# Performance work log

Measured on AMD Instinct MI355X. Metric: run time of the kernel, lower is better.

## Reference

```python
import jax, jax.numpy as jnp
import numpy as np

IN_CH = 512
HID = 512
SCALE = 1.0 / np.sqrt(16.0)  # hard-coded 16**0.5 in source, not sqrt(hidden)


def setup_inputs() -> dict:
    key = jax.random.key(0)
    ks = jax.random.split(key, 9)
    B, T = 8, 2048
    lim = 1.0 / np.sqrt(IN_CH)
    return {
        "q": jax.random.normal(ks[0], (B, T, IN_CH), dtype=jnp.float32),
        "k": jax.random.normal(ks[1], (B, T, IN_CH), dtype=jnp.float32),
        "v": jax.random.normal(ks[2], (B, T, IN_CH), dtype=jnp.float32),
        "Wq": jax.random.uniform(ks[3], (IN_CH, HID), jnp.float32, -lim, lim),
        "bq": jax.random.uniform(ks[4], (HID,), jnp.float32, -lim, lim),
        "Wk": jax.random.uniform(ks[5], (IN_CH, HID), jnp.float32, -lim, lim),
        "bk": jax.random.uniform(ks[6], (HID,), jnp.float32, -lim, lim),
        "Wv": jax.random.uniform(ks[7], (IN_CH, HID), jnp.float32, -lim, lim),
        "bv": jax.random.uniform(ks[8], (HID,), jnp.float32, -lim, lim),
    }


def reference(q, k, v, Wq, bq, Wk, bk, Wv, bv):
    # Linear projections: [B,T,F] @ [F,H] + [H]
    query = jnp.einsum("btf,fh->bth", q, Wq) + bq
    key_p = jnp.einsum("btf,fh->bth", k, Wk) + bk
    value = jnp.einsum("btf,fh->bth", v, Wv) + bv
    # energy: [B,T,T], scaled by fixed 1/sqrt(16)
    energy = jnp.einsum("bth,bsh->bts", query, key_p) * SCALE
    attn = jax.nn.softmax(energy, axis=-1)
    # weighted sum: [B,T,H]
    return jnp.einsum("bts,bsh->bth", attn, value)
```

## Files before the change

### kernel.cpp

```cpp
#include <hip/hip_runtime.h>
#include <stdint.h>

typedef __bf16 bf16;
typedef bf16 bf16x8 __attribute__((ext_vector_type(8)));
typedef float f32x4 __attribute__((ext_vector_type(4)));

#define MFMA(a, b, c) __builtin_amdgcn_mfma_f32_16x16x32_bf16(a, b, c, 0, 0, 0)

#define SCALE_L2E 0.3606737602222409f
#define M0 16.0f

__device__ __forceinline__ void gload_lds16(const void* g, void* l) {
  __builtin_amdgcn_global_load_lds(
      (const __attribute__((address_space(1))) uint32_t*)g,
      (__attribute__((address_space(3))) uint32_t*)l, 16, 0, 0);
}

__global__ void k_wtrans(const float* __restrict__ Wq, const float* __restrict__ Wk,
                         const float* __restrict__ Wv, bf16* __restrict__ Wt) {
  __shared__ float tile[32][33];
  int x = threadIdx.x, y = threadIdx.y;
  int k0 = blockIdx.x * 32, n0 = blockIdx.y * 32, z = blockIdx.z;
  const float* W = (z == 0) ? Wq : (z == 1) ? Wk : Wv;
  for (int j = 0; j < 4; j++)
    tile[y + 8 * j][x] = W[(size_t)(k0 + y + 8 * j) * 512 + n0 + x];
  __syncthreads();
  bf16* o = Wt + (size_t)z * 262144;
  for (int j = 0; j < 4; j++)
    o[(size_t)(n0 + y + 8 * j) * 512 + k0 + x] = (bf16)tile[x][y + 8 * j];
}

__global__ __launch_bounds__(256, 2) void k_proj(
    const float* __restrict__ q, const float* __restrict__ k, const float* __restrict__ v,
    const bf16* __restrict__ Wt, const float* __restrict__ bq, const float* __restrict__ bk,
    const float* __restrict__ bv, bf16* __restrict__ Qp, bf16* __restrict__ Kp,
    bf16* __restrict__ Vtp) {
  int z = blockIdx.z;
  const float* A = (z == 0) ? q : (z == 1) ? k : v;
  const float* bias = (z == 0) ? bq : (z == 1) ? bk : bv;
  const bf16* Bw = Wt + (size_t)z * 262144;

  int m0 = blockIdx.x * 128, n0 = blockIdx.y * 128;
  __shared__ __align__(16) char smem[65536];
  bf16* As = (bf16*)smem;
  bf16* Bs = (bf16*)(smem + 32768);
  bf16* Ts = (bf16*)smem;

  int tid = threadIdx.x;
  int wave = tid >> 6, lane = tid & 63, qr = lane & 15, quad = lane >> 4;
  int wm = (wave >> 1) * 64, wn = (wave & 1) * 64;

  f32x4 acc[4][4];
  for (int mi = 0; mi < 4; mi++)
    for (int ni = 0; ni < 4; ni++) acc[mi][ni] = (f32x4){0.f, 0.f, 0.f, 0.f};

  float4 rx[4], ry[4];

  auto issue = [&](int kk, int buf) {
#pragma unroll
    for (int i = 0; i < 4; i++) {
      int ch = i * 256 + tid, row = ch >> 3, c = ch & 7;
      const float4* src = (const float4*)(A + (size_t)(m0 + row) * 512 + kk + c * 8);
      rx[i] = src[0];
      ry[i] = src[1];
    }
#pragma unroll
    for (int i = 0; i < 4; i++) {
      int ch = i * 256 + tid, row = ch >> 3, c = ch & 7, cs = c ^ (row & 7);
      gload_lds16(Bw + (size_t)(n0 + row) * 512 + kk + cs * 8, &Bs[buf * 8192 + ch * 8]);
    }
  };

  auto writeA = [&](int buf) {
#pragma unroll
    for (int i = 0; i < 4; i++) {
      int ch = i * 256 + tid, row = ch >> 3, c = ch & 7, cs = c ^ (row & 7);
      bf16x8 t;
      t[0] = (bf16)rx[i].x; t[1] = (bf16)rx[i].y; t[2] = (bf16)rx[i].z; t[3] = (bf16)rx[i].w;
      t[4] = (bf16)ry[i].x; t[5] = (bf16)ry[i].y; t[6] = (bf16)ry[i].z; t[7] = (bf16)ry[i].w;
      *(bf16x8*)&As[buf * 8192 + row * 64 + cs * 8] = t;
    }
  };

  auto compute = [&](int buf) {
    bf16* Ab = &As[buf * 8192];
    bf16* Bb = &Bs[buf * 8192];
#pragma unroll
    for (int h = 0; h < 2; h++) {
      bf16x8 af[4], bfv[4];
#pragma unroll
      for (int mi = 0; mi < 4; mi++) {
        int rr = wm + mi * 16 + qr;
        int cc = (h * 4 + quad) ^ (rr & 7);
        af[mi] = *(bf16x8*)&Ab[rr * 64 + cc * 8];
      }
#pragma unroll
      for (int ni = 0; ni < 4; ni++) {
        int rr = wn + ni * 16 + qr;
        int cc = (h * 4 + quad) ^ (rr & 7);
        bfv[ni] = *(bf16x8*)&Bb[rr * 64 + cc * 8];
      }
#pragma unroll
      for (int mi = 0; mi < 4; mi++)
#pragma unroll
        for (int ni = 0; ni < 4; ni++) acc[mi][ni] = MFMA(af[mi], bfv[ni], acc[mi][ni]);
    }
  };

  issue(0, 0);
  writeA(0);
  __syncthreads();

  int cur = 0;
  for (int t = 0; t < 8; t++) {
    if (t < 7) issue((t + 1) * 64, cur ^ 1);
    compute(cur);
    if (t < 7) writeA(cur ^ 1);
    __syncthreads();
    cur ^= 1;
  }

  if (z == 2) {
    for (int ni = 0; ni < 4; ni++) {
      int hcol = wn + ni * 16 + qr;
      float bz = bias[n0 + hcol];
      for (int mi = 0; mi < 4; mi++) {
        int tl = wm + mi * 16 + quad * 4;
        bf16 tmp[4];
        for (int r = 0; r < 4; r++) tmp[r] = (bf16)(acc[mi][ni][r] + bz);
        *(uint64_t*)&Ts[hcol * 136 + tl] = *(uint64_t*)tmp;
      }
    }
    __syncthreads();
    int bb = m0 >> 11, t0l = m0 & 2047;
    for (int i = 0; i < 8; i++) {
      int ch = i * 256 + tid;
      int row = ch >> 4, c = ch & 15;
      *(bf16x8*)(Vtp + (size_t)(bb * 512 + n0 + row) * 2048 + t0l + c * 8) =
          *(bf16x8*)&Ts[row * 136 + c * 8];
    }
  } else {
    bf16* C = (z == 0) ? Qp : Kp;
    float sc = (z == 0) ? SCALE_L2E : 1.0f;
    for (int ni = 0; ni < 4; ni++) {
      int col = n0 + wn + ni * 16 + qr;
      float bz = bias[col];
      for (int mi = 0; mi < 4; mi++) {
        int rbase = m0 + wm + mi * 16 + quad * 4;
        for (int r = 0; r < 4; r++)
          C[(size_t)(rbase + r) * 512 + col] = (bf16)((acc[mi][ni][r] + bz) * sc);
      }
    }
  }
}

__global__ __launch_bounds__(256, 2) void k_qk(const bf16* __restrict__ Qp,
                                               const bf16* __restrict__ Kp,
                                               bf16* __restrict__ P,
                                               float* __restrict__ Lpart) {
  __shared__ bf16 As[2][128 * 64];
  __shared__ bf16 Bs[2][128 * 64];
  int b = blockIdx.z;
  const bf16* A = Qp + (size_t)b * 2048 * 512;
  const bf16* B = Kp + (size_t)b * 2048 * 512;
  bf16* Pb = P + (size_t)b * 2048 * 2048;
  int m0 = blockIdx.x * 128, n0 = blockIdx.y * 128;
  int tid = threadIdx.x;
  int wave = tid >> 6, lane = tid & 63, qr = lane & 15, quad = lane >> 4;
  int wm = (wave >> 1) * 64, wn = (wave & 1) * 64;

  f32x4 acc[4][4];
  for (int mi = 0; mi < 4; mi++)
    for (int ni = 0; ni < 4; ni++) acc[mi][ni] = (f32x4){0.f, 0.f, 0.f, 0.f};

  auto stage = [&](int kk, int buf) {
#pragma unroll
    for (int i = 0; i < 4; i++) {
      int ch = i * 256 + tid, row = ch >> 3, c = ch & 7, cs = c ^ (row & 7);
      gload_lds16(A + (size_t)(m0 + row) * 512 + kk + cs * 8, &As[buf][ch * 8]);
      gload_lds16(B + (size_t)(n0 + row) * 512 + kk + cs * 8, &Bs[buf][ch * 8]);
    }
  };

  auto compute = [&](int buf) {
#pragma unroll
    for (int h = 0; h < 2; h++) {
      bf16x8 af[4], bfv[4];
#pragma unroll
      for (int mi = 0; mi < 4; mi++) {
        int rr = wm + mi * 16 + qr;
        int cc = (h * 4 + quad) ^ (rr & 7);
        af[mi] = *(bf16x8*)&As[buf][rr * 64 + cc * 8];
      }
#pragma unroll
      for (int ni = 0; ni < 4; ni++) {
        int rr = wn + ni * 16 + qr;
        int cc = (h * 4 + quad) ^ (rr & 7);
        bfv[ni] = *(bf16x8*)&Bs[buf][rr * 64 + cc * 8];
      }
#pragma unroll
      for (int mi = 0; mi < 4; mi++)
#pragma unroll
        for (int ni = 0; ni < 4; ni++) acc[mi][ni] = MFMA(af[mi], bfv[ni], acc[mi][ni]);
    }
  };

  stage(0, 0);
  __syncthreads();
  int cur = 0;
  for (int t = 0; t < 8; t++) {
    if (t < 7) stage((t + 1) * 64, cur ^ 1);
    compute(cur);
    __syncthreads();
    cur ^= 1;
  }

  int slice = blockIdx.y * 2 + (wave & 1);
  float* Lp = Lpart + (size_t)slice * 16384 + b * 2048;
  for (int mi = 0; mi < 4; mi++) {
    int rowb = m0 + wm + mi * 16 + quad * 4;
    for (int r = 0; r < 4; r++) {
      float s = 0.f;
      bf16* prow = Pb + (size_t)(rowb + r) * 2048 + n0 + wn + qr;
      for (int ni = 0; ni < 4; ni++) {
        float e = exp2f(acc[mi][ni][r] - M0);
        prow[ni * 16] = (bf16)e;
        s += e;
      }
      s += __shfl_xor(s, 1);
      s += __shfl_xor(s, 2);
      s += __shfl_xor(s, 4);
      s += __shfl_xor(s, 8);
      if (qr == 0) Lp[rowb + r] = s;
    }
  }
}

__global__ __launch_bounds__(256, 2) void k_pv(const bf16* __restrict__ P,
                                               const bf16* __restrict__ Vtp,
                                               const float* __restrict__ Lpart,
                                               float* __restrict__ out) {
  __shared__ bf16 As[2][128 * 64];
  __shared__ bf16 Bs[2][128 * 64];
  int b = blockIdx.z;
  const bf16* A = P + (size_t)b * 2048 * 2048;
  const bf16* B = Vtp + (size_t)b * 512 * 2048;
  int m0 = blockIdx.x * 128, n0 = blockIdx.y * 128;
  int tid = threadIdx.x;
  int wave = tid >> 6, lane = tid & 63, qr = lane & 15, quad = lane >> 4;
  int wm = (wave >> 1) * 64, wn = (wave & 1) * 64;

  float linv_own = 0.f;
  if (tid < 128) {
    float s = 0.f;
    for (int j = 0; j < 32; j++) s += Lpart[(size_t)j * 16384 + b * 2048 + m0 + tid];
    linv_own = 1.0f / s;
  }

  f32x4 acc[4][4];
  for (int mi = 0; mi < 4; mi++)
    for (int ni = 0; ni < 4; ni++) acc[mi][ni] = (f32x4){0.f, 0.f, 0.f, 0.f};

  auto stage = [&](int kk, int buf) {
#pragma unroll
    for (int i = 0; i < 4; i++) {
      int ch = i * 256 + tid, row = ch >> 3, c = ch & 7, cs = c ^ (row & 7);
      gload_lds16(A + (size_t)(m0 + row) * 2048 + kk + cs * 8, &As[buf][ch * 8]);
      gload_lds16(B + (size_t)(n0 + row) * 2048 + kk + cs * 8, &Bs[buf][ch * 8]);
    }
  };

  auto compute = [&](int buf) {
#pragma unroll
    for (int h = 0; h < 2; h++) {
      bf16x8 af[4], bfv[4];
#pragma unroll
      for (int mi = 0; mi < 4; mi++) {
        int rr = wm + mi * 16 + qr;
        int cc = (h * 4 + quad) ^ (rr & 7);
        af[mi] = *(bf16x8*)&As[buf][rr * 64 + cc * 8];
      }
#pragma unroll
      for (int ni = 0; ni < 4; ni++) {
        int rr = wn + ni * 16 + qr;
        int cc = (h * 4 + quad) ^ (rr & 7);
        bfv[ni] = *(bf16x8*)&Bs[buf][rr * 64 + cc * 8];
      }
#pragma unroll
      for (int mi = 0; mi < 4; mi++)
#pragma unroll
        for (int ni = 0; ni < 4; ni++) acc[mi][ni] = MFMA(af[mi], bfv[ni], acc[mi][ni]);
    }
  };

  stage(0, 0);
  __syncthreads();
  int cur = 0;
  for (int t = 0; t < 32; t++) {
    if (t < 31) stage((t + 1) * 64, cur ^ 1);
    compute(cur);
    __syncthreads();
    cur ^= 1;
  }

  float* Linv_s = (float*)&As[0][0];
  if (tid < 128) Linv_s[tid] = linv_own;
  __syncthreads();

  for (int mi = 0; mi < 4; mi++) {
    int rowl = wm + mi * 16 + quad * 4;
    float linv[4];
    for (int r = 0; r < 4; r++) linv[r] = Linv_s[rowl + r];
    for (int ni = 0; ni < 4; ni++) {
      int col = n0 + wn + ni * 16 + qr;
      float* og = out + (size_t)(b * 2048 + m0 + rowl) * 512 + col;
      for (int r = 0; r < 4; r++) og[(size_t)r * 512] = acc[mi][ni][r] * linv[r];
    }
  }
}

extern "C" void kernel_launch(void* const* d_in, const int* in_sizes, int n_in,
                              void* d_out, int out_size, void* d_ws, size_t ws_size,
                              hipStream_t stream) {
  (void)in_sizes; (void)n_in; (void)out_size; (void)ws_size;
  const float* q  = (const float*)d_in[0];
  const float* k  = (const float*)d_in[1];
  const float* v  = (const float*)d_in[2];
  const float* Wq = (const float*)d_in[3];
  const float* bq = (const float*)d_in[4];
  const float* Wk = (const float*)d_in[5];
  const float* bk = (const float*)d_in[6];
  const float* Wv = (const float*)d_in[7];
  const float* bv = (const float*)d_in[8];
  float* out = (float*)d_out;

  char* ws = (char*)d_ws;
  bf16* Wt     = (bf16*)(ws);
  bf16* Qp     = (bf16*)(ws + 1572864);
  bf16* Kp     = (bf16*)(ws + 18350080);
  bf16* Vtp    = (bf16*)(ws + 35127296);
  bf16* P      = (bf16*)(ws + 51904512);
  float* Lpart = (float*)(ws + 119013376);

  k_wtrans<<<dim3(16, 16, 3), dim3(32, 8, 1), 0, stream>>>(Wq, Wk, Wv, Wt);
  k_proj<<<dim3(128, 4, 3), 256, 0, stream>>>(q, k, v, Wt, bq, bk, bv, Qp, Kp, Vtp);
  k_qk<<<dim3(16, 16, 8), 256, 0, stream>>>(Qp, Kp, P, Lpart);
  k_pv<<<dim3(16, 4, 8), 256, 0, stream>>>(P, Vtp, Lpart, out);
}
```

Before: 278.8 us.

## Enlarge QK and PV tiles to 8-wave blocks with explicit barrier-scheduled MFMA phases

The QK^T kernel moves from 128x128 to 256x256 output tiles and the PV kernel from 128x128 to 256x128, each using 512 threads (8 waves) and one block per CU. Each K-step splits into two MFMA phases. They are separated by explicit s_barrier and waitcnt, with sched_barrier and setprio raising wave priority during the matrix work. This replaces __syncthreads. The larger tiles aim to cut redundant global/L2 loads of Q, K, P and V, and the manual scheduling aims to overlap LDS reads, async global-to-LDS copies and MFMA. In exchange, LDS use grows to 128KB and 96KB, occupancy drops to one block per CU, and the PV grid shrinks to 256 blocks, which can hurt latency hiding and tail balance.

```diff
diff --git a/kernel.cpp b/kernel.cpp
--- a/kernel.cpp
+++ b/kernel.cpp
@@ -9,6 +9,12 @@
 
 #define SCALE_L2E 0.3606737602222409f
 #define M0 16.0f
+
+#define WAITVM0 asm volatile("s_waitcnt vmcnt(0)" ::: "memory")
+#define WAITLGKM0 asm volatile("s_waitcnt lgkmcnt(0)" ::: "memory")
+#define SBAR __builtin_amdgcn_s_barrier()
+#define SCHEDB __builtin_amdgcn_sched_barrier(0)
+#define PRIO(x) __builtin_amdgcn_s_setprio(x)
 
 __device__ __forceinline__ void gload_lds16(const void* g, void* l) {
   __builtin_amdgcn_global_load_lds(
@@ -154,74 +160,112 @@
   }
 }
 
-__global__ __launch_bounds__(256, 2) void k_qk(const bf16* __restrict__ Qp,
+__global__ __launch_bounds__(512, 1) void k_qk(const bf16* __restrict__ Qp,
                                                const bf16* __restrict__ Kp,
                                                bf16* __restrict__ P,
                                                float* __restrict__ Lpart) {
-  __shared__ bf16 As[2][128 * 64];
-  __shared__ bf16 Bs[2][128 * 64];
+  __shared__ __align__(16) bf16 S[65536];
   int b = blockIdx.z;
   const bf16* A = Qp + (size_t)b * 2048 * 512;
   const bf16* B = Kp + (size_t)b * 2048 * 512;
   bf16* Pb = P + (size_t)b * 2048 * 2048;
-  int m0 = blockIdx.x * 128, n0 = blockIdx.y * 128;
+  int m0 = blockIdx.x * 256, n0 = blockIdx.y * 256;
   int tid = threadIdx.x;
   int wave = tid >> 6, lane = tid & 63, qr = lane & 15, quad = lane >> 4;
-  int wm = (wave >> 1) * 64, wn = (wave & 1) * 64;
-
-  f32x4 acc[4][4];
-  for (int mi = 0; mi < 4; mi++)
+  int wm = wave >> 2, wn = wave & 3;
+
+  f32x4 acc[8][4];
+  for (int mi = 0; mi < 8; mi++)
     for (int ni = 0; ni < 4; ni++) acc[mi][ni] = (f32x4){0.f, 0.f, 0.f, 0.f};
 
-  auto stage = [&](int kk, int buf) {
-#pragma unroll
-    for (int i = 0; i < 4; i++) {
-      int ch = i * 256 + tid, row = ch >> 3, c = ch & 7, cs = c ^ (row & 7);
-      gload_lds16(A + (size_t)(m0 + row) * 512 + kk + cs * 8, &As[buf][ch * 8]);
-      gload_lds16(B + (size_t)(n0 + row) * 512 + kk + cs * 8, &Bs[buf][ch * 8]);
+  auto stage = [&](int t, int s) {
+    int kk = t * 64;
+    bf16* As_ = S + s * 16384;
+    bf16* Bs_ = S + 32768 + s * 16384;
+#pragma unroll
+    for (int j = 0; j < 4; j++) {
+      int ch = j * 512 + tid, row = ch >> 3, c = ch & 7, cs = c ^ (row & 7);
+      gload_lds16(A + (size_t)(m0 + row) * 512 + kk + cs * 8, As_ + ch * 8);
+    }
+#pragma unroll
+    for (int j = 0; j < 4; j++) {
+      int ch = j * 512 + tid, row = ch >> 3, c = ch & 7, cs = c ^ (row & 7);
+      gload_lds16(B + (size_t)(n0 + row) * 512 + kk + cs * 8, Bs_ + ch * 8);
     }
   };
 
-  auto compute = [&](int buf) {
-#pragma unroll
-    for (int h = 0; h < 2; h++) {
-      bf16x8 af[4], bfv[4];
-#pragma unroll
-      for (int mi = 0; mi < 4; mi++) {
-        int rr = wm + mi * 16 + qr;
-        int cc = (h * 4 + quad) ^ (rr & 7);
-        af[mi] = *(bf16x8*)&As[buf][rr * 64 + cc * 8];
-      }
-#pragma unroll
-      for (int ni = 0; ni < 4; ni++) {
-        int rr = wn + ni * 16 + qr;
-        int cc = (h * 4 + quad) ^ (rr & 7);
-        bfv[ni] = *(bf16x8*)&Bs[buf][rr * 64 + cc * 8];
-      }
+  stage(0, 0);
+  WAITVM0;
+  SBAR;
+
+  for (int t = 0; t < 8; t++) {
+    int cur = t & 1;
+    bf16* As_ = S + cur * 16384;
+    bf16* Bs_ = S + 32768 + cur * 16384;
+
+    if (t < 7) stage(t + 1, cur ^ 1);
+    bf16x8 aF[4][2], bF[4][2];
+#pragma unroll
+    for (int mi = 0; mi < 4; mi++)
+#pragma unroll
+      for (int kk = 0; kk < 2; kk++) {
+        int row = wm * 128 + mi * 16 + qr;
+        aF[mi][kk] = *(bf16x8*)&As_[row * 64 + ((kk * 4 + quad) ^ (row & 7)) * 8];
+      }
+#pragma unroll
+    for (int ni = 0; ni < 4; ni++)
+#pragma unroll
+      for (int kk = 0; kk < 2; kk++) {
+        int row = wn * 64 + ni * 16 + qr;
+        bF[ni][kk] = *(bf16x8*)&Bs_[row * 64 + ((kk * 4 + quad) ^ (row & 7)) * 8];
+      }
+    SBAR;
+    WAITLGKM0;
+    SCHEDB;
+    PRIO(1);
+#pragma unroll
+    for (int kk = 0; kk < 2; kk++)
 #pragma unroll
       for (int mi = 0; mi < 4; mi++)
 #pragma unroll
-        for (int ni = 0; ni < 4; ni++) acc[mi][ni] = MFMA(af[mi], bfv[ni], acc[mi][ni]);
-    }
-  };
-
-  stage(0, 0);
-  __syncthreads();
-  int cur = 0;
-  for (int t = 0; t < 8; t++) {
-    if (t < 7) stage((t + 1) * 64, cur ^ 1);
-    compute(cur);
-    __syncthreads();
-    cur ^= 1;
-  }
-
-  int slice = blockIdx.y * 2 + (wave & 1);
+        for (int ni = 0; ni < 4; ni++)
+          acc[mi][ni] = MFMA(aF[mi][kk], bF[ni][kk], acc[mi][ni]);
+    PRIO(0);
+    SBAR;
+
+#pragma unroll
+    for (int mi = 0; mi < 4; mi++)
+#pragma unroll
+      for (int kk = 0; kk < 2; kk++) {
+        int row = wm * 128 + 64 + mi * 16 + qr;
+        aF[mi][kk] = *(bf16x8*)&As_[row * 64 + ((kk * 4 + quad) ^ (row & 7)) * 8];
+      }
+    SBAR;
+    WAITLGKM0;
+    SCHEDB;
+    PRIO(1);
+#pragma unroll
+    for (int kk = 0; kk < 2; kk++)
+#pragma unroll
+      for (int mi = 0; mi < 4; mi++)
+#pragma unroll
+        for (int ni = 0; ni < 4; ni++)
+          acc[4 + mi][ni] = MFMA(aF[mi][kk], bF[ni][kk], acc[4 + mi][ni]);
+    PRIO(0);
+    WAITVM0;
+    SBAR;
+  }
+
+  int slice = blockIdx.y * 4 + wn;
   float* Lp = Lpart + (size_t)slice * 16384 + b * 2048;
-  for (int mi = 0; mi < 4; mi++) {
-    int rowb = m0 + wm + mi * 16 + quad * 4;
+#pragma unroll
+  for (int mi = 0; mi < 8; mi++) {
+    int rowb = m0 + wm * 128 + mi * 16 + quad * 4;
+#pragma unroll
     for (int r = 0; r < 4; r++) {
       float s = 0.f;
-      bf16* prow = Pb + (size_t)(rowb + r) * 2048 + n0 + wn + qr;
+      bf16* prow = Pb + (size_t)(rowb + r) * 2048 + n0 + wn * 64 + qr;
+#pragma unroll
       for (int ni = 0; ni < 4; ni++) {
         float e = exp2f(acc[mi][ni][r] - M0);
         prow[ni * 16] = (bf16)e;
@@ -236,22 +280,21 @@
   }
 }
 
-__global__ __launch_bounds__(256, 2) void k_pv(const bf16* __restrict__ P,
+__global__ __launch_bounds__(512, 1) void k_pv(const bf16* __restrict__ P,
                                                const bf16* __restrict__ Vtp,
                                                const float* __restrict__ Lpart,
                                                float* __restrict__ out) {
-  __shared__ bf16 As[2][128 * 64];
-  __shared__ bf16 Bs[2][128 * 64];
+  __shared__ __align__(16) bf16 S[49152];
   int b = blockIdx.z;
   const bf16* A = P + (size_t)b * 2048 * 2048;
   const bf16* B = Vtp + (size_t)b * 512 * 2048;
-  int m0 = blockIdx.x * 128, n0 = blockIdx.y * 128;
+  int m0 = blockIdx.x * 256, n0 = blockIdx.y * 128;
   int tid = threadIdx.x;
   int wave = tid >> 6, lane = tid & 63, qr = lane & 15, quad = lane >> 4;
-  int wm = (wave >> 1) * 64, wn = (wave & 1) * 64;
+  int wmi = wave >> 1, wni = wave & 1;
 
   float linv_own = 0.f;
-  if (tid < 128) {
+  if (tid < 256) {
     float s = 0.f;
     for (int j = 0; j < 32; j++) s += Lpart[(size_t)j * 16384 + b * 2048 + m0 + tid];
     linv_own = 1.0f / s;
@@ -261,58 +304,96 @@
   for (int mi = 0; mi < 4; mi++)
     for (int ni = 0; ni < 4; ni++) acc[mi][ni] = (f32x4){0.f, 0.f, 0.f, 0.f};
 
-  auto stage = [&](int kk, int buf) {
-#pragma unroll
-    for (int i = 0; i < 4; i++) {
-      int ch = i * 256 + tid, row = ch >> 3, c = ch & 7, cs = c ^ (row & 7);
-      gload_lds16(A + (size_t)(m0 + row) * 2048 + kk + cs * 8, &As[buf][ch * 8]);
-      gload_lds16(B + (size_t)(n0 + row) * 2048 + kk + cs * 8, &Bs[buf][ch * 8]);
+  auto stage = [&](int t, int s) {
+    int kk = t * 64;
+    bf16* As_ = S + s * 16384;
+    bf16* Bs_ = S + 32768 + s * 8192;
+#pragma unroll
+    for (int j = 0; j < 4; j++) {
+      int ch = j * 512 + tid, row = ch >> 3, c = ch & 7, cs = c ^ (row & 7);
+      gload_lds16(A + (size_t)(m0 + row) * 2048 + kk + cs * 8, As_ + ch * 8);
+    }
+#pragma unroll
+    for (int j = 0; j < 2; j++) {
+      int ch = j * 512 + tid, row = ch >> 3, c = ch & 7, cs = c ^ (row & 7);
+      gload_lds16(B + (size_t)(n0 + row) * 2048 + kk + cs * 8, Bs_ + ch * 8);
     }
   };
 
-  auto compute = [&](int buf) {
-#pragma unroll
-    for (int h = 0; h < 2; h++) {
-      bf16x8 af[4], bfv[4];
-#pragma unroll
-      for (int mi = 0; mi < 4; mi++) {
-        int rr = wm + mi * 16 + qr;
-        int cc = (h * 4 + quad) ^ (rr & 7);
-        af[mi] = *(bf16x8*)&As[buf][rr * 64 + cc * 8];
-      }
-#pragma unroll
-      for (int ni = 0; ni < 4; ni++) {
-        int rr = wn + ni * 16 + qr;
-        int cc = (h * 4 + quad) ^ (rr & 7);
-        bfv[ni] = *(bf16x8*)&Bs[buf][rr * 64 + cc * 8];
-      }
-#pragma unroll
-      for (int mi = 0; mi < 4; mi++)
-#pragma unroll
-        for (int ni = 0; ni < 4; ni++) acc[mi][ni] = MFMA(af[mi], bfv[ni], acc[mi][ni]);
-    }
-  };
-
   stage(0, 0);
-  __syncthreads();
-  int cur = 0;
+  WAITVM0;
+  SBAR;
+
   for (int t = 0; t < 32; t++) {
-    if (t < 31) stage((t + 1) * 64, cur ^ 1);
-    compute(cur);
-    __syncthreads();
-    cur ^= 1;
-  }
-
-  float* Linv_s = (float*)&As[0][0];
-  if (tid < 128) Linv_s[tid] = linv_own;
-  __syncthreads();
-
+    int cur = t & 1;
+    bf16* As_ = S + cur * 16384;
+    bf16* Bs_ = S + 32768 + cur * 8192;
+
+    if (t < 31) stage(t + 1, cur ^ 1);
+    bf16x8 aF[2][2], bF[4][2];
+#pragma unroll
+    for (int mi = 0; mi < 2; mi++)
+#pragma unroll
+      for (int kk = 0; kk < 2; kk++) {
+        int row = wmi * 64 + mi * 16 + qr;
+        aF[mi][kk] = *(bf16x8*)&As_[row * 64 + ((kk * 4 + quad) ^ (row & 7)) * 8];
+      }
+#pragma unroll
+    for (int ni = 0; ni < 4; ni++)
+#pragma unroll
+      for (int kk = 0; kk < 2; kk++) {
+        int row = wni * 64 + ni * 16 + qr;
+        bF[ni][kk] = *(bf16x8*)&Bs_[row * 64 + ((kk * 4 + quad) ^ (row & 7)) * 8];
+      }
+    SBAR;
+    WAITLGKM0;
+    SCHEDB;
+    PRIO(1);
+#pragma unroll
+    for (int kk = 0; kk < 2; kk++)
+#pragma unroll
+      for (int mi = 0; mi < 2; mi++)
+#pragma unroll
+        for (int ni = 0; ni < 4; ni++)
+          acc[mi][ni] = MFMA(aF[mi][kk], bF[ni][kk], acc[mi][ni]);
+    PRIO(0);
+    SBAR;
+
+#pragma unroll
+    for (int mi = 0; mi < 2; mi++)
+#pragma unroll
+      for (int kk = 0; kk < 2; kk++) {
+        int row = wmi * 64 + 32 + mi * 16 + qr;
+        aF[mi][kk] = *(bf16x8*)&As_[row * 64 + ((kk * 4 + quad) ^ (row & 7)) * 8];
+      }
+    SBAR;
+    WAITLGKM0;
+    SCHEDB;
+    PRIO(1);
+#pragma unroll
+    for (int kk = 0; kk < 2; kk++)
+#pragma unroll
+      for (int mi = 0; mi < 2; mi++)
+#pragma unroll
+        for (int ni = 0; ni < 4; ni++)
+          acc[2 + mi][ni] = MFMA(aF[mi][kk], bF[ni][kk], acc[2 + mi][ni]);
+    PRIO(0);
+    WAITVM0;
+    SBAR;
+  }
+
+  float* Linv_s = (float*)S;
+  if (tid < 256) Linv_s[tid] = linv_own;
+  SBAR;
+
+#pragma unroll
   for (int mi = 0; mi < 4; mi++) {
-    int rowl = wm + mi * 16 + quad * 4;
+    int rowl = wmi * 64 + mi * 16 + quad * 4;
     float linv[4];
     for (int r = 0; r < 4; r++) linv[r] = Linv_s[rowl + r];
+#pragma unroll
     for (int ni = 0; ni < 4; ni++) {
-      int col = n0 + wn + ni * 16 + qr;
+      int col = n0 + wni * 64 + ni * 16 + qr;
       float* og = out + (size_t)(b * 2048 + m0 + rowl) * 512 + col;
       for (int r = 0; r < 4; r++) og[(size_t)r * 512] = acc[mi][ni][r] * linv[r];
     }
@@ -344,6 +425,6 @@
 
   k_wtrans<<<dim3(16, 16, 3), dim3(32, 8, 1), 0, stream>>>(Wq, Wk, Wv, Wt);
   k_proj<<<dim3(128, 4, 3), 256, 0, stream>>>(q, k, v, Wt, bq, bk, bv, Qp, Kp, Vtp);
-  k_qk<<<dim3(16, 16, 8), 256, 0, stream>>>(Qp, Kp, P, Lpart);
-  k_pv<<<dim3(16, 4, 8), 256, 0, stream>>>(P, Vtp, Lpart, out);
-}
+  k_qk<<<dim3(8, 8, 8), 512, 0, stream>>>(Qp, Kp, P, Lpart);
+  k_pv<<<dim3(8, 4, 8), 512, 0, stream>>>(P, Vtp, Lpart, out);
+}
```

Measured after the change: 267.7 us. -4.0%, faster.
